# Performance work log

Measured on AMD Instinct MI355X. Metric: run time of the kernel, lower is better.

The kernel has to match this reference:

```python
import jax, jax.numpy as jnp
import numpy as np

PERIMETER = 2.0 * np.pi  # cyclicity of phi
STD = 1.0                # kernel bandwidth (init kwarg std)


def _sq_dists(p):
    # p: [B, N, 2] -> squared euclidean distances [B, N, N]
    sqnorm = jnp.sum(p * p, axis=2)                    # [B, N]
    dot = jnp.einsum('bnd,bmd->bnm', p, p)             # [B, N, N]
    return sqnorm[:, :, None] + sqnorm[:, None, :] - 2.0 * dot


def _distances(phi, eta, alpha=1.0):
    # squared distances with 2*pi cyclicity on phi:
    # min over phi shifted by half-perimeter ((a+b)/2 - |a-b|/2 == min(a,b))
    p1 = jnp.stack((eta * alpha, phi % PERIMETER), axis=2)
    d1 = _sq_dists(p1)
    p2 = jnp.stack((eta * alpha, (phi + PERIMETER / 2) % PERIMETER), axis=2)
    d2 = _sq_dists(p2)
    return jnp.minimum(d1, d2)


def setup_inputs() -> dict:
    key = jax.random.key(0)
    k1, k2, k3 = jax.random.split(key, 3)
    B, N = 16, 2048
    e = jax.random.normal(k1, (B, N), dtype=jnp.float32)
    phi = jax.random.normal(k2, (B, N), dtype=jnp.float32)
    eta = jax.random.normal(k3, (B, N), dtype=jnp.float32)
    return {"e": e, "phi": phi, "eta": eta}


def reference(e, phi, eta):
    # compute_kernel: gaussian adjacency on cyclic squared distances
    adj = jnp.exp(-_distances(phi, eta) / STD)          # [B, N, N]
    # order_pooling: sort nodes by degree (row sums), descending
    degree = jnp.sum(adj, axis=2)                       # [B, N]
    order = jnp.argsort(-degree, axis=1)                # [B, N] int
    # order_matrix: permute rows then columns of adjacency
    adj_o = jnp.take_along_axis(adj, order[:, :, None], axis=1)
    adj_o = jnp.take_along_axis(adj_o, order[:, None, :], axis=2)
    # order_vector: permute per-node features
    e_o = jnp.take_along_axis(e, order, axis=1)
    phi_o = jnp.take_along_axis(phi, order, axis=1)
    eta_o = jnp.take_along_axis(eta, order, axis=1)
    return (adj_o, e_o, phi_o, eta_o)
```

## Files before the change

kernel.cpp:

```cpp
#include <hip/hip_runtime.h>
#include <hip/hip_bf16.h>

#define BN 16
#define NN 2048

#define P_F  6.28318530717958647692f
#define HP_F 3.14159265358979323846f

__device__ __forceinline__ float pmod(float x) {
    float r = fmodf(x, P_F);
    return (r < 0.0f) ? r + P_F : r;
}

__device__ __forceinline__ float adjval(float xi, float a1, float a2,
                                        float xj, float b1, float b2) {
    float dx = xi - xj;
    float t  = dx * dx;
    float u  = a1 - b1;
    float v  = a2 - b2;
    float d1 = fmaf(u, u, t);
    float d2 = fmaf(v, v, t);
    return __expf(-fminf(d1, d2));
}

__global__ __launch_bounds__(256) void k_degree(const float* __restrict__ phi,
                                                const float* __restrict__ eta,
                                                float* __restrict__ degree) {
#pragma clang fp contract(off)
    int blk = blockIdx.x;
    int b   = blk >> 7;
    int r0  = (blk & 127) << 4;

    __shared__ float se[NN], sp1[NN], sp2[NN], sn1[NN], sn2[NN];
    const float* pb = phi + (size_t)b * NN;
    const float* eb = eta + (size_t)b * NN;
    for (int j = threadIdx.x; j < NN; j += 256) {
        float p  = pb[j];
        float x  = eb[j];
        float p1 = pmod(p);
        float p2 = pmod(p + HP_F);
        se[j]  = x;
        sp1[j] = p1;
        sp2[j] = p2;
        sn1[j] = x * x + p1 * p1;
        sn2[j] = x * x + p2 * p2;
    }
    __syncthreads();

    int row16  = threadIdx.x >> 4;
    int lane16 = threadIdx.x & 15;
    int i = r0 + row16;

    float xi  = se[i],  p1i = sp1[i], p2i = sp2[i];
    float n1i = sn1[i], n2i = sn2[i];

    int jbase = lane16 * 128;

    auto elem = [&](int j) -> float {
        float me   = xi * se[j];
        float dot1 = me + p1i * sp1[j];
        float dot2 = me + p2i * sp2[j];
        float d1   = (n1i + sn1[j]) - 2.0f * dot1;
        float d2   = (n2i + sn2[j]) - 2.0f * dot2;
        float dmin = fminf(d1, d2);
        return (float)exp(-(double)dmin);
    };

    float r[8];
    #pragma unroll
    for (int t = 0; t < 8; ++t) r[t] = elem(jbase + t);
    for (int i8 = 8; i8 < 128; i8 += 8) {
        #pragma unroll
        for (int t = 0; t < 8; ++t) r[t] = r[t] + elem(jbase + i8 + t);
    }
    float rr = ((r[0] + r[1]) + (r[2] + r[3])) + ((r[4] + r[5]) + (r[6] + r[7]));

    #pragma unroll
    for (int m = 1; m <= 8; m <<= 1) {
        rr = rr + __shfl_xor(rr, m, 64);
    }
    if (lane16 == 0) degree[(size_t)b * NN + i] = rr;
}

__global__ __launch_bounds__(1024) void k_sort(const float* __restrict__ degree,
                                               int* __restrict__ order) {
    int b = blockIdx.x;
    __shared__ float key[NN];
    __shared__ int   idx[NN];
    for (int i = threadIdx.x; i < NN; i += 1024) {
        key[i] = degree[(size_t)b * NN + i];
        idx[i] = i;
    }
    __syncthreads();

    for (int k = 2; k <= NN; k <<= 1) {
        for (int j = k >> 1; j > 0; j >>= 1) {
            for (int i = threadIdx.x; i < NN; i += 1024) {
                int ixj = i ^ j;
                if (ixj > i) {
                    float ka = key[i], kb = key[ixj];
                    int   ia = idx[i], ib = idx[ixj];
                    bool before = (ka > kb) || (ka == kb && ia < ib);
                    bool revSeg = ((i & k) != 0);
                    bool doSwap = revSeg ? before : !before;
                    if (doSwap) {
                        key[i] = kb; key[ixj] = ka;
                        idx[i] = ib; idx[ixj] = ia;
                    }
                }
            }
            __syncthreads();
        }
    }
    for (int i = threadIdx.x; i < NN; i += 1024) {
        order[(size_t)b * NN + i] = idx[i];
    }
}

__global__ __launch_bounds__(256) void k_perm(const float* __restrict__ e,
                                              const float* __restrict__ phi,
                                              const float* __restrict__ eta,
                                              const int* __restrict__ order,
                                              float* __restrict__ out_e,
                                              float* __restrict__ out_phi,
                                              float* __restrict__ out_eta) {
    int t = blockIdx.x * 256 + threadIdx.x;
    int b = t / NN;
    int o = order[t];
    size_t src = (size_t)b * NN + o;
    out_e[t]   = e[src];
    out_phi[t] = phi[src];
    out_eta[t] = eta[src];
}

#define ROWS 8
__global__ __launch_bounds__(256) void k_adj(const float* __restrict__ phi_o,
                                             const float* __restrict__ eta_o,
                                             float* __restrict__ adj) {
    int blk = blockIdx.x;
    int b   = blk / (NN / ROWS);
    int r0  = (blk % (NN / ROWS)) * ROWS;

    __shared__ float sx[NN], s1[NN], s2[NN];
    const float* pb = phi_o + (size_t)b * NN;
    const float* eb = eta_o + (size_t)b * NN;
    for (int j = threadIdx.x; j < NN; j += 256) {
        float p = pb[j];
        sx[j] = eb[j];
        s1[j] = pmod(p);
        s2[j] = pmod(p + HP_F);
    }
    __syncthreads();

    float* base = adj + ((size_t)b * NN + r0) * NN;
    for (int r = 0; r < ROWS; ++r) {
        int i = r0 + r;
        float xi = sx[i], a1 = s1[i], a2 = s2[i];
        #pragma unroll
        for (int p = 0; p < 2; ++p) {
            int j0 = p * 1024 + threadIdx.x * 4;
            float4 xv = *reinterpret_cast<const float4*>(&sx[j0]);
            float4 y1 = *reinterpret_cast<const float4*>(&s1[j0]);
            float4 y2 = *reinterpret_cast<const float4*>(&s2[j0]);
            float4 o;
            o.x = adjval(xi, a1, a2, xv.x, y1.x, y2.x);
            o.y = adjval(xi, a1, a2, xv.y, y1.y, y2.y);
            o.z = adjval(xi, a1, a2, xv.z, y1.z, y2.z);
            o.w = adjval(xi, a1, a2, xv.w, y1.w, y2.w);
            *reinterpret_cast<float4*>(&base[(size_t)r * NN + j0]) = o;
        }
    }
}

extern "C" void kernel_launch(void* const* d_in, const int* in_sizes, int n_in,
                              void* d_out, int out_size, void* d_ws, size_t ws_size,
                              hipStream_t stream) {
    const float* e   = (const float*)d_in[0];
    const float* phi = (const float*)d_in[1];
    const float* eta = (const float*)d_in[2];

    float* adj     = (float*)d_out;
    float* out_e   = adj + (size_t)BN * NN * NN;
    float* out_phi = out_e + (size_t)BN * NN;
    float* out_eta = out_phi + (size_t)BN * NN;

    float* degree = (float*)d_ws;
    int*   order  = (int*)((char*)d_ws + (size_t)BN * NN * sizeof(float));

    k_degree<<<BN * (NN / 16), 256, 0, stream>>>(phi, eta, degree);
    k_sort<<<BN, 1024, 0, stream>>>(degree, order);
    k_perm<<<(BN * NN) / 256, 256, 0, stream>>>(e, phi, eta, order,
                                                out_e, out_phi, out_eta);
    k_adj<<<BN * (NN / ROWS), 256, 0, stream>>>(out_phi, out_eta, adj);
}
```

Before: 448.9 us.

## Replace bitonic sort with rank counting, pad LDS, use inline double exp

The per-batch bitonic sort and separate permutation kernel are replaced by a rank-by-counting kernel. Each thread counts how many degrees beat its own, using the same tie-breaking rule, and scatters its features directly to that rank. The degree kernel pads its shared arrays to avoid bank conflicts across the 16 lanes that stride by 128, and swaps libm double exp for an inline Taylor-polynomial double exp. This cuts one launch and the serialized sort, at the cost of O(N^2) comparisons per batch and a hand-written exp that needs to match the library result closely enough to keep the ordering.

```diff
diff --git a/kernel.cpp b/kernel.cpp
--- a/kernel.cpp
+++ b/kernel.cpp
@@ -6,6 +6,9 @@
 
 #define P_F  6.28318530717958647692f
 #define HP_F 3.14159265358979323846f
+
+#define PIDX(j) ((j) + ((j) >> 7))
+#define PN (NN + 16)
 
 __device__ __forceinline__ float pmod(float x) {
     float r = fmodf(x, P_F);
@@ -23,6 +26,30 @@
     return __expf(-fminf(d1, d2));
 }
 
+__device__ __forceinline__ double expd_fast(double x) {
+    const double L2E   = 1.44269504088896338700e+00;
+    const double LN2HI = 6.93147180369123816490e-01;
+    const double LN2LO = 1.90821492927058770002e-10;
+    double n  = rint(x * L2E);
+    double r  = fma(n, -LN2HI, x);
+    r         = fma(n, -LN2LO, r);
+    double h  = 2.5052108385441720e-08;
+    h = fma(h, r, 2.7557319223985888e-07);
+    h = fma(h, r, 2.7557319223985893e-06);
+    h = fma(h, r, 2.4801587301587302e-05);
+    h = fma(h, r, 1.9841269841269841e-04);
+    h = fma(h, r, 1.3888888888888889e-03);
+    h = fma(h, r, 8.3333333333333332e-03);
+    h = fma(h, r, 4.1666666666666664e-02);
+    h = fma(h, r, 1.6666666666666666e-01);
+    h = fma(h, r, 0.5);
+    double q = fma(h, r, 1.0);
+    double e = fma(q, r, 1.0);
+    long long ll = (long long)n;
+    double s = __longlong_as_double((ll + 1023) << 52);
+    return e * s;
+}
+
 __global__ __launch_bounds__(256) void k_degree(const float* __restrict__ phi,
                                                 const float* __restrict__ eta,
                                                 float* __restrict__ degree) {
@@ -31,7 +58,7 @@
     int b   = blk >> 7;
     int r0  = (blk & 127) << 4;
 
-    __shared__ float se[NN], sp1[NN], sp2[NN], sn1[NN], sn2[NN];
+    __shared__ float se[PN], sp1[PN], sp2[PN], sn1[PN], sn2[PN];
     const float* pb = phi + (size_t)b * NN;
     const float* eb = eta + (size_t)b * NN;
     for (int j = threadIdx.x; j < NN; j += 256) {
@@ -39,36 +66,39 @@
         float x  = eb[j];
         float p1 = pmod(p);
         float p2 = pmod(p + HP_F);
-        se[j]  = x;
-        sp1[j] = p1;
-        sp2[j] = p2;
-        sn1[j] = x * x + p1 * p1;
-        sn2[j] = x * x + p2 * p2;
+        int jj = PIDX(j);
+        se[jj]  = x;
+        sp1[jj] = p1;
+        sp2[jj] = p2;
+        sn1[jj] = x * x + p1 * p1;
+        sn2[jj] = x * x + p2 * p2;
     }
     __syncthreads();
 
     int row16  = threadIdx.x >> 4;
     int lane16 = threadIdx.x & 15;
-    int i = r0 + row16;
-
-    float xi  = se[i],  p1i = sp1[i], p2i = sp2[i];
-    float n1i = sn1[i], n2i = sn2[i];
-
-    int jbase = lane16 * 128;
-
-    auto elem = [&](int j) -> float {
-        float me   = xi * se[j];
-        float dot1 = me + p1i * sp1[j];
-        float dot2 = me + p2i * sp2[j];
-        float d1   = (n1i + sn1[j]) - 2.0f * dot1;
-        float d2   = (n2i + sn2[j]) - 2.0f * dot2;
+    int i  = r0 + row16;
+    int ii = PIDX(i);
+
+    float xi  = se[ii],  p1i = sp1[ii], p2i = sp2[ii];
+    float n1i = sn1[ii], n2i = sn2[ii];
+
+    int jbase = lane16 * 129;
+
+    auto elem = [&](int jj) -> float {
+        float me   = xi * se[jj];
+        float dot1 = me + p1i * sp1[jj];
+        float dot2 = me + p2i * sp2[jj];
+        float d1   = (n1i + sn1[jj]) - 2.0f * dot1;
+        float d2   = (n2i + sn2[jj]) - 2.0f * dot2;
         float dmin = fminf(d1, d2);
-        return (float)exp(-(double)dmin);
+        return (float)expd_fast(-(double)dmin);
     };
 
     float r[8];
     #pragma unroll
     for (int t = 0; t < 8; ++t) r[t] = elem(jbase + t);
+    #pragma unroll 2
     for (int i8 = 8; i8 < 128; i8 += 8) {
         #pragma unroll
         for (int t = 0; t < 8; ++t) r[t] = r[t] + elem(jbase + i8 + t);
@@ -82,55 +112,40 @@
     if (lane16 == 0) degree[(size_t)b * NN + i] = rr;
 }
 
-__global__ __launch_bounds__(1024) void k_sort(const float* __restrict__ degree,
-                                               int* __restrict__ order) {
-    int b = blockIdx.x;
-    __shared__ float key[NN];
-    __shared__ int   idx[NN];
-    for (int i = threadIdx.x; i < NN; i += 1024) {
-        key[i] = degree[(size_t)b * NN + i];
-        idx[i] = i;
-    }
-    __syncthreads();
-
-    for (int k = 2; k <= NN; k <<= 1) {
-        for (int j = k >> 1; j > 0; j >>= 1) {
-            for (int i = threadIdx.x; i < NN; i += 1024) {
-                int ixj = i ^ j;
-                if (ixj > i) {
-                    float ka = key[i], kb = key[ixj];
-                    int   ia = idx[i], ib = idx[ixj];
-                    bool before = (ka > kb) || (ka == kb && ia < ib);
-                    bool revSeg = ((i & k) != 0);
-                    bool doSwap = revSeg ? before : !before;
-                    if (doSwap) {
-                        key[i] = kb; key[ixj] = ka;
-                        idx[i] = ib; idx[ixj] = ia;
-                    }
-                }
-            }
-            __syncthreads();
-        }
-    }
-    for (int i = threadIdx.x; i < NN; i += 1024) {
-        order[(size_t)b * NN + i] = idx[i];
-    }
-}
-
-__global__ __launch_bounds__(256) void k_perm(const float* __restrict__ e,
+__global__ __launch_bounds__(256) void k_rank(const float* __restrict__ degree,
+                                              const float* __restrict__ e,
                                               const float* __restrict__ phi,
                                               const float* __restrict__ eta,
-                                              const int* __restrict__ order,
                                               float* __restrict__ out_e,
                                               float* __restrict__ out_phi,
                                               float* __restrict__ out_eta) {
-    int t = blockIdx.x * 256 + threadIdx.x;
-    int b = t / NN;
-    int o = order[t];
-    size_t src = (size_t)b * NN + o;
-    out_e[t]   = e[src];
-    out_phi[t] = phi[src];
-    out_eta[t] = eta[src];
+    int blk = blockIdx.x;
+    int b   = blk >> 3;
+    int r0  = (blk & 7) << 8;
+    int i   = r0 + threadIdx.x;
+
+    __shared__ float sdeg[NN];
+    const float* db = degree + (size_t)b * NN;
+    for (int j = threadIdx.x; j < NN; j += 256) sdeg[j] = db[j];
+    __syncthreads();
+
+    float di = sdeg[i];
+    int c0 = 0, c1 = 0, c2 = 0, c3 = 0;
+    #pragma unroll 4
+    for (int j = 0; j < NN; j += 4) {
+        float d0 = sdeg[j], d1v = sdeg[j + 1], d2v = sdeg[j + 2], d3v = sdeg[j + 3];
+        c0 += (d0  > di) || (d0  == di && (j    ) < i);
+        c1 += (d1v > di) || (d1v == di && (j + 1) < i);
+        c2 += (d2v > di) || (d2v == di && (j + 2) < i);
+        c3 += (d3v > di) || (d3v == di && (j + 3) < i);
+    }
+    int rank = (c0 + c1) + (c2 + c3);
+
+    size_t src = (size_t)b * NN + i;
+    size_t dst = (size_t)b * NN + rank;
+    out_e[dst]   = e[src];
+    out_phi[dst] = phi[src];
+    out_eta[dst] = eta[src];
 }
 
 #define ROWS 8
@@ -185,11 +200,9 @@
     float* out_eta = out_phi + (size_t)BN * NN;
 
     float* degree = (float*)d_ws;
-    int*   order  = (int*)((char*)d_ws + (size_t)BN * NN * sizeof(float));
 
     k_degree<<<BN * (NN / 16), 256, 0, stream>>>(phi, eta, degree);
-    k_sort<<<BN, 1024, 0, stream>>>(degree, order);
-    k_perm<<<(BN * NN) / 256, 256, 0, stream>>>(e, phi, eta, order,
-                                                out_e, out_phi, out_eta);
+    k_rank<<<BN * 8, 256, 0, stream>>>(degree, e, phi, eta,
+                                       out_e, out_phi, out_eta);
     k_adj<<<BN * (NN / ROWS), 256, 0, stream>>>(out_phi, out_eta, adj);
 }
```

New measurement: 400.2 us. 1.12x faster.
